# Kernel tuning notes

Hardware: AMD Instinct MI355X
Metric: run time of the kernel (lower is better)

## Reference

```python
import jax, jax.numpy as jnp
import numpy as np

FEATURE_DIM = 768
NUM_HEADS = 16
HEAD_DIM = FEATURE_DIM // NUM_HEADS
SCALE = HEAD_DIM ** -0.5


def setup_inputs() -> dict:
    key = jax.random.key(0)
    ks = jax.random.split(key, 9)
    B, N, C = 4, 2048, FEATURE_DIM
    s = 0.02
    return {
        "x": jax.random.normal(ks[0], (B, N, C), dtype=jnp.float32),
        "wq": jax.random.normal(ks[1], (C, C), dtype=jnp.float32) * s,
        "bq": jax.random.normal(ks[2], (C,), dtype=jnp.float32) * s,
        "wk": jax.random.normal(ks[3], (C, C), dtype=jnp.float32) * s,
        "bk": jax.random.normal(ks[4], (C,), dtype=jnp.float32) * s,
        "wv": jax.random.normal(ks[5], (C, C), dtype=jnp.float32) * s,
        "bv": jax.random.normal(ks[6], (C,), dtype=jnp.float32) * s,
        "wo": jax.random.normal(ks[7], (C, C), dtype=jnp.float32) * s,
        "bo": jax.random.normal(ks[8], (C,), dtype=jnp.float32) * s,
    }


def reference(x, wq, bq, wk, bk, wv, bv, wo, bo):
    B, N, C = x.shape
    H, D = NUM_HEADS, HEAD_DIM
    # Linear layers use weight of shape (out, in): y = x @ W.T + b
    def proj(w, b):
        return (jnp.einsum("bnc,dc->bnd", x, w) + b).reshape(B, N, H, D).transpose(0, 2, 1, 3)
    q = proj(wq, bq)  # [B,H,N,D]
    k = proj(wk, bk)
    v = proj(wv, bv)
    attn = jnp.einsum("bhnd,bhmd->bhnm", q, k) * SCALE
    attn = jax.nn.softmax(attn, axis=-1)  # dropout = identity (eval mode)
    y = jnp.einsum("bhnm,bhmd->bhnd", attn, v).transpose(0, 2, 1, 3).reshape(B, N, C)
    y = y + x
    out = jnp.einsum("bnc,dc->bnd", y, wo) + bo
    out = out + y
    return out + x
```

## Files before the change

### kernel.cpp

```cpp
#include <hip/hip_runtime.h>
#include <hip/hip_bf16.h>

#define B_ 4
#define N_ 2048
#define C_ 768
#define H_ 16
#define D_ 48
#define SCALE_ 0.14433756729740643f
#define LOG2E_ 1.44269504088896f

using bf16 = __hip_bfloat16;
using bf16x8 = __attribute__((ext_vector_type(8))) short;
using f32x4  = __attribute__((ext_vector_type(4))) float;
using f32x16 = __attribute__((ext_vector_type(16))) float;
using u32x2  = __attribute__((ext_vector_type(2))) unsigned int;
using u32x4  = __attribute__((ext_vector_type(4))) unsigned int;

__device__ __forceinline__ unsigned short f2b(float f) {
  bf16 h = __float2bfloat16(f);
  return *reinterpret_cast<unsigned short*>(&h);
}
__device__ __forceinline__ unsigned int pack2(float lo, float hi) {
  return (unsigned int)f2b(lo) | ((unsigned int)f2b(hi) << 16);
}
__device__ __forceinline__ unsigned int pk2(float lo, float hi) {
  unsigned int r;
  asm("v_cvt_pk_bf16_f32 %0, %1, %2" : "=v"(r) : "v"(lo), "v"(hi));
  return r;
}
__device__ __forceinline__ float b2f(unsigned short us) {
  return __builtin_bit_cast(float, (unsigned)us << 16);
}
__device__ __forceinline__ uint4 ld8f_cvt(const float* p) {
  float4 a = *reinterpret_cast<const float4*>(p);
  float4 b = *reinterpret_cast<const float4*>(p + 4);
  uint4 u;
  u.x = pack2(a.x, a.y); u.y = pack2(a.z, a.w);
  u.z = pack2(b.x, b.y); u.w = pack2(b.z, b.w);
  return u;
}
__device__ __forceinline__ void gload_lds16(const bf16* g, bf16* l) {
  __builtin_amdgcn_global_load_lds(
      (const __attribute__((address_space(1))) unsigned int*)g,
      (__attribute__((address_space(3))) unsigned int*)l, 16, 0, 0);
}

__global__ __launch_bounds__(256) void cvt_bf16(
    const float* __restrict__ x,  const float* __restrict__ wq,
    const float* __restrict__ wk, const float* __restrict__ wv,
    const float* __restrict__ wo,
    bf16* __restrict__ xb, bf16* __restrict__ wqkvb, bf16* __restrict__ wob,
    bf16* __restrict__ vfp)
{
  const int job = blockIdx.y;
  if (job == 5) {
    for (int u = blockIdx.x * 256 + threadIdx.x; u < 64 * 128 * 32;
         u += gridDim.x * 256) {
      const int m5i = u & 15, hb = (u >> 4) & 1, n4 = (u >> 5) & 127,
                bh = u >> 12;
      const short fill = (m5i == 0) ? (short)0x3F80 : (short)0;
      const bf16x8 o = {fill, fill, fill, fill, fill, fill, fill, fill};
      *(bf16x8*)(vfp + (size_t)bh * 131072 + n4 * 1024 + 512 + hb * 256 +
                 (16 + m5i) * 8) = o;
    }
    return;
  }
  const float* src; bf16* dst; int n;
  if (job == 0)      { src = x;  dst = xb;              n = B_ * N_ * C_; }
  else if (job == 1) { src = wq; dst = wqkvb;           n = C_ * C_; }
  else if (job == 2) { src = wk; dst = wqkvb + C_ * C_; n = C_ * C_; }
  else if (job == 3) { src = wv; dst = wqkvb + 2 * C_ * C_; n = C_ * C_; }
  else               { src = wo; dst = wob;             n = C_ * C_; }
  const int stride = gridDim.x * 256 * 8;
  for (int i = (blockIdx.x * 256 + threadIdx.x) * 8; i < n; i += stride)
    *(uint4*)(dst + i) = ld8f_cvt(src + i);
}

__global__ __launch_bounds__(256) void gemm_qkv(
    const bf16* __restrict__ A, const bf16* __restrict__ Bw,
    const float* __restrict__ bq, const float* __restrict__ bk,
    const float* __restrict__ bv,
    bf16* __restrict__ Q, bf16* __restrict__ K, bf16* __restrict__ Vf)
{
  __shared__ __align__(16) bf16 As[128 * 64];
  __shared__ __align__(16) bf16 Bs[128 * 64];

  const int lid  = blockIdx.x + 18 * blockIdx.y;
  const int nlid = (lid & 7) * 144 + (lid >> 3);
  const int bx = nlid % 18, by = nlid / 18;

  const int tid  = threadIdx.x;
  const int lane = tid & 63, wid = tid >> 6;
  const int wm = (wid >> 1) * 64, wn = (wid & 1) * 64;
  const int row0 = by * 128, col0 = bx * 128;
  const int mb = lane & 15, g4 = lane >> 4;
  const int srow = lane >> 3;
  const int schunk = (lane & 7) ^ (srow & 7);
  const int z = bx / 6;

  f32x4 acc[4][4];
#pragma unroll
  for (int i = 0; i < 4; ++i)
#pragma unroll
    for (int j = 0; j < 4; ++j) acc[i][j] = (f32x4){0.f, 0.f, 0.f, 0.f};

  auto kloop = [&](bool swapped) {
    for (int k0 = 0; k0 < C_; k0 += 64) {
#pragma unroll
      for (int t = 0; t < 4; ++t) {
        const int rt = wid * 32 + t * 8;
        gload_lds16(A  + (size_t)(row0 + rt + srow) * C_ + k0 + schunk * 8,
                    As + rt * 64);
        gload_lds16(Bw + (size_t)(col0 + rt + srow) * C_ + k0 + schunk * 8,
                    Bs + rt * 64);
      }
      __syncthreads();
#pragma unroll
      for (int ks = 0; ks < 2; ++ks) {
        const int kchunk = ks * 4 + g4;
        bf16x8 af[4], bfr[4];
#pragma unroll
        for (int i = 0; i < 4; ++i) {
          const int row = wm + i * 16 + mb;
          af[i] = *(const bf16x8*)(As + row * 64 + (kchunk ^ (row & 7)) * 8);
        }
#pragma unroll
        for (int j = 0; j < 4; ++j) {
          const int col = wn + j * 16 + mb;
          bfr[j] = *(const bf16x8*)(Bs + col * 64 + (kchunk ^ (col & 7)) * 8);
        }
        if (swapped) {
#pragma unroll
          for (int i = 0; i < 4; ++i)
#pragma unroll
            for (int j = 0; j < 4; ++j)
              acc[i][j] = __builtin_amdgcn_mfma_f32_16x16x32_bf16(bfr[j], af[i], acc[i][j], 0, 0, 0);
        } else {
#pragma unroll
          for (int i = 0; i < 4; ++i)
#pragma unroll
            for (int j = 0; j < 4; ++j)
              acc[i][j] = __builtin_amdgcn_mfma_f32_16x16x32_bf16(af[i], bfr[j], acc[i][j], 0, 0, 0);
        }
      }
      __syncthreads();
    }
  };

  const int b_ = row0 >> 11;
  const int nb = (row0 & (N_ - 1)) + wm;
  if (z < 2) {
    kloop(true);
    const float* bias = (z == 0) ? bq : bk;
    bf16* dst = (z == 0) ? Q : K;
    const float sc = (z == 0) ? (SCALE_ * LOG2E_) : 1.0f;
#pragma unroll
    for (int j = 0; j < 4; ++j) {
      const int c = col0 - z * 768 + wn + j * 16 + g4 * 4;
      const int h = c / D_, d0 = c % D_;
      const float4 bb = *(const float4*)(bias + c);
      bf16* slabp = dst + (size_t)(b_ * H_ + h) * (N_ * D_);
      const int dpart = (d0 >> 4) * 512 + ((d0 >> 3) & 1) * 256 + (d0 & 7);
#pragma unroll
      for (int i = 0; i < 4; ++i) {
        const int n = nb + i * 16 + mb;
        u32x2 wv;
        wv.x = pk2((acc[i][j][0] + bb.x) * sc, (acc[i][j][1] + bb.y) * sc);
        wv.y = pk2((acc[i][j][2] + bb.z) * sc, (acc[i][j][3] + bb.w) * sc);
        *(u32x2*)(slabp + (n >> 5) * 1536 + dpart + (n & 31) * 8) = wv;
      }
    }
  } else {
    kloop(false);
#pragma unroll
    for (int j = 0; j < 4; ++j) {
      const int oo = col0 - 2 * 768 + wn + j * 16 + mb;
      const int h = oo / D_, d = oo % D_;
      const float bb = bv[oo];
      bf16* slabp = Vf + (size_t)(b_ * H_ + h) * (N_ * 64);
      const int dpart = (d >> 5) * 512 + ((g4 >> 1) * 32 + (d & 31)) * 8 +
                        (g4 & 1) * 4;
#pragma unroll
      for (int i = 0; i < 4; ++i) {
        u32x2 wv;
        wv.x = pk2(acc[i][j][0] + bb, acc[i][j][1] + bb);
        wv.y = pk2(acc[i][j][2] + bb, acc[i][j][3] + bb);
        *(u32x2*)(slabp + ((nb >> 4) + i) * 1024 + dpart) = wv;
      }
    }
  }
}

__global__ __launch_bounds__(256, 2) void attn_mfma(
    const bf16* __restrict__ Qf, const bf16* __restrict__ Kf,
    const bf16* __restrict__ Vf, const float* __restrict__ x,
    bf16* __restrict__ Yb)
{
  __shared__ __align__(16) bf16 Ls[2 * 7168];

  const int tid  = threadIdx.x;
  const int lane = tid & 63, wid = tid >> 6;
  const int m5 = lane & 31, hi = lane >> 5;
  const int bh = blockIdx.x;
  const int b_ = bh >> 4, h = bh & 15;
  const int q0 = blockIdx.y * 256 + wid * 64;
  const size_t slab  = (size_t)bh * (N_ * D_);
  const size_t slabV = (size_t)bh * (N_ * 64);

  bf16x8 qfA[3], qfB[3];
  const int kgq = q0 >> 5;
#pragma unroll
  for (int kc = 0; kc < 3; ++kc) {
    qfA[kc] = *(const bf16x8*)(Qf + slab + (size_t)(((kgq * 3 + kc) * 64) + lane) * 8);
    qfB[kc] = *(const bf16x8*)(Qf + slab + (size_t)((((kgq + 1) * 3 + kc) * 64) + lane) * 8);
  }

  f32x16 zf;
#pragma unroll
  for (int r = 0; r < 16; ++r) zf[r] = 0.f;

  f32x16 OA[2], OB[2];
#pragma unroll
  for (int dt = 0; dt < 2; ++dt)
#pragma unroll
    for (int r = 0; r < 16; ++r) { OA[dt][r] = 0.f; OB[dt][r] = 0.f; }

  const bf16* kb = Kf + slab  + (size_t)lane * 8;
  const bf16* vb = Vf + slabV + (size_t)lane * 8;
  auto stage = [&](int t, int buf) {
    bf16* dstb = Ls + buf * 7168;
    const bf16* kt = kb + (size_t)t * 3072;
    const bf16* vt = vb + (size_t)t * 4096;
    for (int c = wid; c < 14; c += 4) {
      if (c < 6) gload_lds16(kt + c * 512, dstb + c * 512);
      else       gload_lds16(vt + (c - 6) * 512, dstb + c * 512);
    }
  };

  auto smpv = [&](f32x16& S, f32x16& O0, f32x16& O1, bf16x8 (&vA)[2][2]) {
#pragma unroll
    for (int r = 0; r < 16; ++r)
      S[r] = __builtin_amdgcn_exp2f(S[r]);
#pragma unroll
    for (int ks = 0; ks < 2; ++ks) {
      const int qa = ks * 2;
      const unsigned A0 = pk2(S[4 * qa + 0], S[4 * qa + 1]);
      const unsigned A1 = pk2(S[4 * qa + 2], S[4 * qa + 3]);
      const unsigned B0 = pk2(S[4 * qa + 4], S[4 * qa + 5]);
      const unsigned B1 = pk2(S[4 * qa + 6], S[4 * qa + 7]);
      const u32x2 r02 = __builtin_amdgcn_permlane32_swap(A0, B0, false, false);
      const u32x2 r13 = __builtin_amdgcn_permlane32_swap(A1, B1, false, false);
      u32x4 pw;
      pw.x = r02.x; pw.y = r13.x; pw.z = r02.y; pw.w = r13.y;
      const bf16x8 pb = (bf16x8)pw;
      O0 = __builtin_amdgcn_mfma_f32_32x32x16_bf16(vA[ks][0], pb, O0, 0, 0, 0);
      O1 = __builtin_amdgcn_mfma_f32_32x32x16_bf16(vA[ks][1], pb, O1, 0, 0, 0);
    }
  };

  auto sub = [&](int buf, int s) {
    const bf16* Lb = Ls + buf * 7168 + (size_t)lane * 8;
    bf16x8 kf[3], vA[2][2];
#pragma unroll
    for (int kc = 0; kc < 3; ++kc)
      kf[kc] = *(const bf16x8*)(Lb + (s * 3 + kc) * 512);
#pragma unroll
    for (int ks = 0; ks < 2; ++ks)
#pragma unroll
      for (int dt = 0; dt < 2; ++dt)
        vA[ks][dt] = *(const bf16x8*)(Lb + (6 + s * 4 + ks * 2 + dt) * 512);
    {
      f32x16 S;
      S = __builtin_amdgcn_mfma_f32_32x32x16_bf16(kf[0], qfA[0], zf, 0, 0, 0);
      S = __builtin_amdgcn_mfma_f32_32x32x16_bf16(kf[1], qfA[1], S, 0, 0, 0);
      S = __builtin_amdgcn_mfma_f32_32x32x16_bf16(kf[2], qfA[2], S, 0, 0, 0);
      smpv(S, OA[0], OA[1], vA);
    }
    {
      f32x16 S;
      S = __builtin_amdgcn_mfma_f32_32x32x16_bf16(kf[0], qfB[0], zf, 0, 0, 0);
      S = __builtin_amdgcn_mfma_f32_32x32x16_bf16(kf[1], qfB[1], S, 0, 0, 0);
      S = __builtin_amdgcn_mfma_f32_32x32x16_bf16(kf[2], qfB[2], S, 0, 0, 0);
      smpv(S, OB[0], OB[1], vA);
    }
  };

  stage(0, 0);
  __syncthreads();
  int buf = 0;
#pragma unroll 1
  for (int t = 0; t < 32; ++t) {
    if (t + 1 < 32) stage(t + 1, buf ^ 1);
    sub(buf, 0);
    sub(buf, 1);
    __syncthreads();
    buf ^= 1;
  }

  auto epi = [&](const f32x16& O0, const f32x16& O1, int qbase) {
    const float lf = O1[8];
    const unsigned lu = __builtin_bit_cast(unsigned, lf);
    const u32x2 lsw = __builtin_amdgcn_permlane32_swap(lu, lu, false, false);
    const float Lv = __builtin_bit_cast(float, lsw.x);
    const float inv = 1.f / Lv;
    const int n = qbase + m5;
    const size_t rowoff = ((size_t)(b_ * N_ + n)) * C_ + h * D_;
#pragma unroll
    for (int qq = 0; qq < 4; ++qq) {
      const size_t off = rowoff + 8 * qq + 4 * hi;
      const float4 xr = *(const float4*)(x + off);
      u32x2 wv;
      wv.x = pk2(O0[4 * qq + 0] * inv + xr.x, O0[4 * qq + 1] * inv + xr.y);
      wv.y = pk2(O0[4 * qq + 2] * inv + xr.z, O0[4 * qq + 3] * inv + xr.w);
      *(u32x2*)(Yb + off) = wv;
    }
#pragma unroll
    for (int qq = 0; qq < 2; ++qq) {
      const size_t off = rowoff + 32 + 8 * qq + 4 * hi;
      const float4 xr = *(const float4*)(x + off);
      u32x2 wv;
      wv.x = pk2(O1[4 * qq + 0] * inv + xr.x, O1[4 * qq + 1] * inv + xr.y);
      wv.y = pk2(O1[4 * qq + 2] * inv + xr.z, O1[4 * qq + 3] * inv + xr.w);
      *(u32x2*)(Yb + off) = wv;
    }
  };
  epi(OA[0], OA[1], q0);
  epi(OB[0], OB[1], q0 + 32);
}

__global__ __launch_bounds__(256) void gemm_out(
    const bf16* __restrict__ Yb, const bf16* __restrict__ Bw,
    const float* __restrict__ bo, const float* __restrict__ x,
    float* __restrict__ out)
{
  __shared__ __align__(16) bf16 As[64 * 64];
  __shared__ __align__(16) bf16 Bs[128 * 64];

  const int lid  = blockIdx.x + 6 * blockIdx.y;
  const int nlid = (lid & 7) * 96 + (lid >> 3);
  const int bx = nlid % 6, by = nlid / 6;

  const int tid  = threadIdx.x;
  const int lane = tid & 63, wid = tid >> 6;
  const int wm = (wid >> 1) * 32, wn = (wid & 1) * 64;
  const int row0 = by * 64, col0 = bx * 128;
  const int mb = lane & 15, g4 = lane >> 4;
  const int srow = lane >> 3;
  const int schunk = (lane & 7) ^ (srow & 7);

  f32x4 acc[2][4];
#pragma unroll
  for (int i = 0; i < 2; ++i)
#pragma unroll
    for (int j = 0; j < 4; ++j) acc[i][j] = (f32x4){0.f, 0.f, 0.f, 0.f};

  for (int k0 = 0; k0 < C_; k0 += 64) {
#pragma unroll
    for (int t = 0; t < 2; ++t) {
      const int rt = wid * 16 + t * 8;
      gload_lds16(Yb + (size_t)(row0 + rt + srow) * C_ + k0 + schunk * 8,
                  As + rt * 64);
    }
#pragma unroll
    for (int t = 0; t < 4; ++t) {
      const int rt = wid * 32 + t * 8;
      gload_lds16(Bw + (size_t)(col0 + rt + srow) * C_ + k0 + schunk * 8,
                  Bs + rt * 64);
    }
    __syncthreads();
#pragma unroll
    for (int ks = 0; ks < 2; ++ks) {
      const int kchunk = ks * 4 + g4;
      bf16x8 af[2], bfr[4];
#pragma unroll
      for (int i = 0; i < 2; ++i) {
        const int row = wm + i * 16 + mb;
        af[i] = *(const bf16x8*)(As + row * 64 + (kchunk ^ (row & 7)) * 8);
      }
#pragma unroll
      for (int j = 0; j < 4; ++j) {
        const int col = wn + j * 16 + mb;
        bfr[j] = *(const bf16x8*)(Bs + col * 64 + (kchunk ^ (col & 7)) * 8);
      }
#pragma unroll
      for (int i = 0; i < 2; ++i)
#pragma unroll
        for (int j = 0; j < 4; ++j)
          acc[i][j] = __builtin_amdgcn_mfma_f32_16x16x32_bf16(bfr[j], af[i], acc[i][j], 0, 0, 0);
    }
    __syncthreads();
  }

#pragma unroll
  for (int j = 0; j < 4; ++j) {
    const int o0 = col0 + wn + j * 16 + g4 * 4;
    const float4 bb = *(const float4*)(bo + o0);
#pragma unroll
    for (int i = 0; i < 2; ++i) {
      const int r = row0 + wm + i * 16 + mb;
      const size_t off = (size_t)r * C_ + o0;
      const u32x2 yv = *(const u32x2*)(Yb + off);
      const float4 xr = *(const float4*)(x + off);
      float4 ov;
      ov.x = acc[i][j][0] + bb.x + b2f((unsigned short)(yv.x & 0xffff)) + xr.x;
      ov.y = acc[i][j][1] + bb.y + b2f((unsigned short)(yv.x >> 16))    + xr.y;
      ov.z = acc[i][j][2] + bb.z + b2f((unsigned short)(yv.y & 0xffff)) + xr.z;
      ov.w = acc[i][j][3] + bb.w + b2f((unsigned short)(yv.y >> 16))    + xr.w;
      *(float4*)(out + off) = ov;
    }
  }
}

extern "C" void kernel_launch(void* const* d_in, const int* in_sizes, int n_in,
                              void* d_out, int out_size, void* d_ws, size_t ws_size,
                              hipStream_t stream)
{
  const float* x  = (const float*)d_in[0];
  const float* wq = (const float*)d_in[1];
  const float* bq = (const float*)d_in[2];
  const float* wk = (const float*)d_in[3];
  const float* bk = (const float*)d_in[4];
  const float* wv = (const float*)d_in[5];
  const float* bv = (const float*)d_in[6];
  const float* wo = (const float*)d_in[7];
  const float* bo = (const float*)d_in[8];
  float* out = (float*)d_out;

  const size_t nEl  = (size_t)B_ * N_ * C_;
  const size_t wEl  = (size_t)C_ * C_;
  const size_t vfEl = (size_t)B_ * H_ * N_ * 64;
  bf16* Q     = (bf16*)d_ws;
  bf16* K     = Q + nEl;
  bf16* Vf    = K + nEl;
  bf16* Yb    = Vf + vfEl;
  bf16* xb    = Yb + nEl;
  bf16* wqkvb = xb + nEl;
  bf16* wob   = wqkvb + 3 * wEl;

  dim3 gcvt(768, 6);
  cvt_bf16<<<gcvt, dim3(256), 0, stream>>>(x, wq, wk, wv, wo, xb, wqkvb, wob, Vf);

  dim3 gqkv(18, 64);
  gemm_qkv<<<gqkv, dim3(256), 0, stream>>>(xb, wqkvb, bq, bk, bv, Q, K, Vf);

  dim3 gattn(B_ * H_, N_ / 256);
  attn_mfma<<<gattn, dim3(256), 0, stream>>>(Q, K, Vf, x, Yb);

  dim3 gout(6, 128);
  gemm_out<<<gout, dim3(256), 0, stream>>>(Yb, wob, bo, x, out);
}
```

Measured before the change: 225.0 us.

## Halve attention queries per wave, raise occupancy, add MFMA priority hints

The attention kernel now gives each wave 32 query rows instead of 64, which halves the accumulator registers, and it doubles the grid in the query dimension. The launch bound moves from 2 to 4 blocks per CU. s_setprio is placed around the MFMA groups, and the residual is read from the bf16 copy of x instead of the fp32 one. The aim is more waves in flight to hide exp and LDS latency, but each K/V tile loaded into LDS is now reused by half as many queries, which doubles K/V traffic, and the residual picks up bf16 rounding.

```diff
diff --git a/kernel.cpp b/kernel.cpp
--- a/kernel.cpp
+++ b/kernel.cpp
@@ -191,9 +191,9 @@
   }
 }
 
-__global__ __launch_bounds__(256, 2) void attn_mfma(
+__global__ __launch_bounds__(256, 4) void attn_mfma(
     const bf16* __restrict__ Qf, const bf16* __restrict__ Kf,
-    const bf16* __restrict__ Vf, const float* __restrict__ x,
+    const bf16* __restrict__ Vf, const bf16* __restrict__ xb,
     bf16* __restrict__ Yb)
 {
   __shared__ __align__(16) bf16 Ls[2 * 7168];
@@ -203,27 +203,25 @@
   const int m5 = lane & 31, hi = lane >> 5;
   const int bh = blockIdx.x;
   const int b_ = bh >> 4, h = bh & 15;
-  const int q0 = blockIdx.y * 256 + wid * 64;
+  const int q0 = blockIdx.y * 128 + wid * 32;
   const size_t slab  = (size_t)bh * (N_ * D_);
   const size_t slabV = (size_t)bh * (N_ * 64);
 
-  bf16x8 qfA[3], qfB[3];
+  bf16x8 qf[3];
   const int kgq = q0 >> 5;
 #pragma unroll
-  for (int kc = 0; kc < 3; ++kc) {
-    qfA[kc] = *(const bf16x8*)(Qf + slab + (size_t)(((kgq * 3 + kc) * 64) + lane) * 8);
-    qfB[kc] = *(const bf16x8*)(Qf + slab + (size_t)((((kgq + 1) * 3 + kc) * 64) + lane) * 8);
-  }
+  for (int kc = 0; kc < 3; ++kc)
+    qf[kc] = *(const bf16x8*)(Qf + slab + (size_t)(((kgq * 3 + kc) * 64) + lane) * 8);
 
   f32x16 zf;
 #pragma unroll
   for (int r = 0; r < 16; ++r) zf[r] = 0.f;
 
-  f32x16 OA[2], OB[2];
+  f32x16 Oacc[2];
 #pragma unroll
   for (int dt = 0; dt < 2; ++dt)
 #pragma unroll
-    for (int r = 0; r < 16; ++r) { OA[dt][r] = 0.f; OB[dt][r] = 0.f; }
+    for (int r = 0; r < 16; ++r) Oacc[dt][r] = 0.f;
 
   const bf16* kb = Kf + slab  + (size_t)lane * 8;
   const bf16* vb = Vf + slabV + (size_t)lane * 8;
@@ -237,7 +235,23 @@
     }
   };
 
-  auto smpv = [&](f32x16& S, f32x16& O0, f32x16& O1, bf16x8 (&vA)[2][2]) {
+  auto sub = [&](int buf, int s) {
+    const bf16* Lb = Ls + buf * 7168 + (size_t)lane * 8;
+    bf16x8 kf[3], vA[2][2];
+#pragma unroll
+    for (int kc = 0; kc < 3; ++kc)
+      kf[kc] = *(const bf16x8*)(Lb + (s * 3 + kc) * 512);
+#pragma unroll
+    for (int ks = 0; ks < 2; ++ks)
+#pragma unroll
+      for (int dt = 0; dt < 2; ++dt)
+        vA[ks][dt] = *(const bf16x8*)(Lb + (6 + s * 4 + ks * 2 + dt) * 512);
+    f32x16 S;
+    __builtin_amdgcn_s_setprio(1);
+    S = __builtin_amdgcn_mfma_f32_32x32x16_bf16(kf[0], qf[0], zf, 0, 0, 0);
+    S = __builtin_amdgcn_mfma_f32_32x32x16_bf16(kf[1], qf[1], S, 0, 0, 0);
+    S = __builtin_amdgcn_mfma_f32_32x32x16_bf16(kf[2], qf[2], S, 0, 0, 0);
+    __builtin_amdgcn_s_setprio(0);
 #pragma unroll
     for (int r = 0; r < 16; ++r)
       S[r] = __builtin_amdgcn_exp2f(S[r]);
@@ -253,35 +267,10 @@
       u32x4 pw;
       pw.x = r02.x; pw.y = r13.x; pw.z = r02.y; pw.w = r13.y;
       const bf16x8 pb = (bf16x8)pw;
-      O0 = __builtin_amdgcn_mfma_f32_32x32x16_bf16(vA[ks][0], pb, O0, 0, 0, 0);
-      O1 = __builtin_amdgcn_mfma_f32_32x32x16_bf16(vA[ks][1], pb, O1, 0, 0, 0);
-    }
-  };
-
-  auto sub = [&](int buf, int s) {
-    const bf16* Lb = Ls + buf * 7168 + (size_t)lane * 8;
-    bf16x8 kf[3], vA[2][2];
-#pragma unroll
-    for (int kc = 0; kc < 3; ++kc)
-      kf[kc] = *(const bf16x8*)(Lb + (s * 3 + kc) * 512);
-#pragma unroll
-    for (int ks = 0; ks < 2; ++ks)
-#pragma unroll
-      for (int dt = 0; dt < 2; ++dt)
-        vA[ks][dt] = *(const bf16x8*)(Lb + (6 + s * 4 + ks * 2 + dt) * 512);
-    {
-      f32x16 S;
-      S = __builtin_amdgcn_mfma_f32_32x32x16_bf16(kf[0], qfA[0], zf, 0, 0, 0);
-      S = __builtin_amdgcn_mfma_f32_32x32x16_bf16(kf[1], qfA[1], S, 0, 0, 0);
-      S = __builtin_amdgcn_mfma_f32_32x32x16_bf16(kf[2], qfA[2], S, 0, 0, 0);
-      smpv(S, OA[0], OA[1], vA);
-    }
-    {
-      f32x16 S;
-      S = __builtin_amdgcn_mfma_f32_32x32x16_bf16(kf[0], qfB[0], zf, 0, 0, 0);
-      S = __builtin_amdgcn_mfma_f32_32x32x16_bf16(kf[1], qfB[1], S, 0, 0, 0);
-      S = __builtin_amdgcn_mfma_f32_32x32x16_bf16(kf[2], qfB[2], S, 0, 0, 0);
-      smpv(S, OB[0], OB[1], vA);
+      __builtin_amdgcn_s_setprio(1);
+      Oacc[0] = __builtin_amdgcn_mfma_f32_32x32x16_bf16(vA[ks][0], pb, Oacc[0], 0, 0, 0);
+      Oacc[1] = __builtin_amdgcn_mfma_f32_32x32x16_bf16(vA[ks][1], pb, Oacc[1], 0, 0, 0);
+      __builtin_amdgcn_s_setprio(0);
     }
   };
 
@@ -297,35 +286,36 @@
     buf ^= 1;
   }
 
-  auto epi = [&](const f32x16& O0, const f32x16& O1, int qbase) {
-    const float lf = O1[8];
-    const unsigned lu = __builtin_bit_cast(unsigned, lf);
-    const u32x2 lsw = __builtin_amdgcn_permlane32_swap(lu, lu, false, false);
-    const float Lv = __builtin_bit_cast(float, lsw.x);
-    const float inv = 1.f / Lv;
-    const int n = qbase + m5;
-    const size_t rowoff = ((size_t)(b_ * N_ + n)) * C_ + h * D_;
-#pragma unroll
-    for (int qq = 0; qq < 4; ++qq) {
-      const size_t off = rowoff + 8 * qq + 4 * hi;
-      const float4 xr = *(const float4*)(x + off);
-      u32x2 wv;
-      wv.x = pk2(O0[4 * qq + 0] * inv + xr.x, O0[4 * qq + 1] * inv + xr.y);
-      wv.y = pk2(O0[4 * qq + 2] * inv + xr.z, O0[4 * qq + 3] * inv + xr.w);
-      *(u32x2*)(Yb + off) = wv;
-    }
-#pragma unroll
-    for (int qq = 0; qq < 2; ++qq) {
-      const size_t off = rowoff + 32 + 8 * qq + 4 * hi;
-      const float4 xr = *(const float4*)(x + off);
-      u32x2 wv;
-      wv.x = pk2(O1[4 * qq + 0] * inv + xr.x, O1[4 * qq + 1] * inv + xr.y);
-      wv.y = pk2(O1[4 * qq + 2] * inv + xr.z, O1[4 * qq + 3] * inv + xr.w);
-      *(u32x2*)(Yb + off) = wv;
-    }
-  };
-  epi(OA[0], OA[1], q0);
-  epi(OB[0], OB[1], q0 + 32);
+  const float lf = Oacc[1][8];
+  const unsigned lu = __builtin_bit_cast(unsigned, lf);
+  const u32x2 lsw = __builtin_amdgcn_permlane32_swap(lu, lu, false, false);
+  const float Lv = __builtin_bit_cast(float, lsw.x);
+  const float inv = 1.f / Lv;
+
+  const int n = q0 + m5;
+  const size_t rowoff = ((size_t)(b_ * N_ + n)) * C_ + h * D_;
+#pragma unroll
+  for (int qq = 0; qq < 4; ++qq) {
+    const size_t off = rowoff + 8 * qq + 4 * hi;
+    const u32x2 xv = *(const u32x2*)(xb + off);
+    u32x2 wv;
+    wv.x = pk2(Oacc[0][4 * qq + 0] * inv + b2f((unsigned short)(xv.x & 0xffff)),
+               Oacc[0][4 * qq + 1] * inv + b2f((unsigned short)(xv.x >> 16)));
+    wv.y = pk2(Oacc[0][4 * qq + 2] * inv + b2f((unsigned short)(xv.y & 0xffff)),
+               Oacc[0][4 * qq + 3] * inv + b2f((unsigned short)(xv.y >> 16)));
+    *(u32x2*)(Yb + off) = wv;
+  }
+#pragma unroll
+  for (int qq = 0; qq < 2; ++qq) {
+    const size_t off = rowoff + 32 + 8 * qq + 4 * hi;
+    const u32x2 xv = *(const u32x2*)(xb + off);
+    u32x2 wv;
+    wv.x = pk2(Oacc[1][4 * qq + 0] * inv + b2f((unsigned short)(xv.x & 0xffff)),
+               Oacc[1][4 * qq + 1] * inv + b2f((unsigned short)(xv.x >> 16)));
+    wv.y = pk2(Oacc[1][4 * qq + 2] * inv + b2f((unsigned short)(xv.y & 0xffff)),
+               Oacc[1][4 * qq + 3] * inv + b2f((unsigned short)(xv.y >> 16)));
+    *(u32x2*)(Yb + off) = wv;
+  }
 }
 
 __global__ __launch_bounds__(256) void gemm_out(
@@ -443,8 +433,8 @@
   dim3 gqkv(18, 64);
   gemm_qkv<<<gqkv, dim3(256), 0, stream>>>(xb, wqkvb, bq, bk, bv, Q, K, Vf);
 
-  dim3 gattn(B_ * H_, N_ / 256);
-  attn_mfma<<<gattn, dim3(256), 0, stream>>>(Q, K, Vf, x, Yb);
+  dim3 gattn(B_ * H_, N_ / 128);
+  attn_mfma<<<gattn, dim3(256), 0, stream>>>(Q, K, Vf, xb, Yb);
 
   dim3 gout(6, 128);
   gemm_out<<<gout, dim3(256), 0, stream>>>(Yb, wob, bo, x, out);
```

Result: no change. 224.3 us (-0.3%).
